# Kernel optimization log

Hardware: AMD Instinct MI355X
Metric: run time of the kernel (lower is better)

## Reference

```python
import jax
import jax.numpy as jnp
from jax import lax
import numpy as np

# module hyperparameters (match init_kwargs)
IN_C, OUT_C = 32, 64
K, STRIDE, PAD, DIL = 3, 1, 1, 1
GRID_SIZE, ORDER = 5, 3
GRID_LO, GRID_HI = -1.0, 1.0
SCALE_SPLINE = 1.0
EPS = 1e-8


def _knot_grid():
    # grid = arange(-order, grid_size+order+1) * h + lo ; length = grid_size + 2*order + 1 = 12
    h = (GRID_HI - GRID_LO) / GRID_SIZE
    return jnp.arange(-ORDER, GRID_SIZE + ORDER + 1, dtype=jnp.float32) * h + GRID_LO


def _bspline_bases(x):
    """Cox-de Boor recursion. x: (N, P) -> bases: (N, P, GRID_SIZE+ORDER)."""
    grid = _knot_grid()
    xe = x[..., None]  # (N, P, 1)
    bases = ((xe >= grid[:-1]) & (xe < grid[1:])).astype(x.dtype)  # (N, P, 11)
    for k in range(1, ORDER + 1):
        left_den = jnp.maximum(grid[k:-1] - grid[:-(k + 1)], EPS)
        right_den = jnp.maximum(grid[k + 1:] - grid[1:-k], EPS)
        bases = ((xe - grid[:-(k + 1)]) / left_den * bases[..., :-1]
                 + (grid[k + 1:] - xe) / right_den * bases[..., 1:])
    return bases  # (N, P, 8)


def setup_inputs() -> dict:
    key = jax.random.key(0)
    k1, k2, k3 = jax.random.split(key, 3)
    x = jax.random.normal(k1, (4, IN_C, 56, 56), dtype=jnp.float32)
    base_weight = jax.random.normal(k2, (OUT_C, IN_C, K, K), dtype=jnp.float32) * 0.05
    spline_weight = jax.random.normal(k3, (OUT_C, IN_C * K * K, GRID_SIZE + ORDER), dtype=jnp.float32) * 0.05
    spline_scaler = jnp.ones((OUT_C,), dtype=jnp.float32)
    return {"x": x, "base_weight": base_weight,
            "spline_weight": spline_weight, "spline_scaler": spline_scaler}


def reference(x, base_weight, spline_weight, spline_scaler):
    B, C, H, W = x.shape
    pad = [(PAD, PAD), (PAD, PAD)]
    # base path: conv2d -> SiLU
    base_conv = lax.conv_general_dilated(
        x, base_weight, window_strides=(STRIDE, STRIDE), padding=pad,
        rhs_dilation=(DIL, DIL), dimension_numbers=("NCHW", "OIHW", "NCHW"))
    base_out = jax.nn.silu(base_conv)

    # unfold: (B, C*K*K, oh, ow) with torch Unfold channel ordering (c, kh, kw)
    patches = lax.conv_general_dilated_patches(
        x, filter_shape=(K, K), window_strides=(STRIDE, STRIDE), padding=pad,
        rhs_dilation=(DIL, DIL))
    oh, ow = patches.shape[2], patches.shape[3]
    num_patches = oh * ow
    # (B*num_patches, C*K*K)
    pf = patches.reshape(B, C * K * K, num_patches).transpose(0, 2, 1).reshape(-1, C * K * K)

    bases = _bspline_bases(pf)  # (N, P, F)
    # contract patch-dim and basis-dim against spline weights
    spl = jnp.einsum("npf,opf->no", bases, spline_weight) * spline_scaler  # (N, O)
    spl = spl.reshape(B, num_patches, OUT_C).transpose(0, 2, 1).reshape(B, OUT_C, oh, ow)
    return base_out + SCALE_SPLINE * spl
```

## Files before the change

### kernel.cpp

```cpp
#include <hip/hip_runtime.h>
#include <math.h>


typedef __attribute__((ext_vector_type(8))) short bf16x8;
typedef __attribute__((ext_vector_type(4))) float f32x4;

#define MFMA16(a, b, c) __builtin_amdgcn_mfma_f32_16x16x32_bf16((a), (b), (c), 0, 0, 0)

__device__ __forceinline__ unsigned short f2bf(float f) {
    unsigned u = __builtin_bit_cast(unsigned, f);
    u = (u + 0x7fffu + ((u >> 16) & 1u)) >> 16;
    return (unsigned short)u;
}

__device__ __forceinline__ void eval_bases(float v, float bs[8]) {
    #pragma unroll
    for (int i = 0; i < 8; ++i) bs[i] = 0.0f;
    float t = (v + 2.2f) * 2.5f;
    if (t >= 0.0f && t < 11.0f) {
        int j = (int)t;
        if (j > 10) j = 10;
        float knot = (float)(j - 3) * 0.4f - 1.0f;
        float u  = (v - knot) * 2.5f;
        float um = 1.0f - u;
        float u2 = u * u, u3 = u2 * u;
        const float s6 = 1.0f / 6.0f;
        float w0 = um * um * um * s6;
        float w1 = (3.0f * u3 - 6.0f * u2 + 4.0f) * s6;
        float w2 = (-3.0f * u3 + 3.0f * u2 + 3.0f * u + 1.0f) * s6;
        float w3 = u3 * s6;
        int i0 = j - 3;
        if (i0 >= 0)               bs[i0]     = w0;
        if (i0 + 1 >= 0 && i0 < 7) bs[i0 + 1] = w1;
        if (i0 + 2 >= 0 && i0 < 6) bs[i0 + 2] = w2;
        if (i0 + 3 <= 7)           bs[i0 + 3] = w3;
    }
}

__global__ __launch_bounds__(256)
void cvt_swz_kernel(const float* __restrict__ ws, const float* __restrict__ wb,
                    unsigned short* __restrict__ wst, unsigned short* __restrict__ wbt) {
    int i = blockIdx.x * 256 + threadIdx.x;
    if (i < 147456) {
        int j = i & 7, l = (i >> 3) & 63, t = i >> 9;
        int S = t % 72, nq = t / 72;
        int oc = nq * 16 + (l & 15);
        int k  = S * 32 + (l >> 4) * 8 + j;
        wst[i] = f2bf(ws[oc * 2304 + k]);
    } else {
        int i2 = i - 147456;
        if (i2 < 18432) {
            int j = i2 & 7, l = (i2 >> 3) & 63, t = i2 >> 9;
            int s = t % 9, nq = t / 9;
            int oc = nq * 16 + (l & 15);
            int k  = s * 32 + (l >> 4) * 8 + j;
            wbt[i2] = f2bf(wb[oc * 288 + k]);
        }
    }
}

__global__ __launch_bounds__(512)
void kan_mfma_kernel(const float* __restrict__ x,
                     const float* __restrict__ sc,
                     const unsigned short* __restrict__ wst,
                     const unsigned short* __restrict__ wbt,
                     float* __restrict__ out) {
    __shared__ unsigned short smem[24832];
    unsigned short* sb    = smem;
    unsigned short* patch = smem + 15360;

    const int tid = threadIdx.x;
    const int bx  = blockIdx.x;
    const int b   = bx / 98;
    const int r   = bx - b * 98;
    const int ty  = r / 7;
    const int tx  = r - ty * 7;
    const int h0  = ty * 4, w0 = tx * 8;

    const int lane = tid & 63;
    const int wv   = tid >> 6;
    const int nq   = wv & 3;
    const int kh   = wv >> 2;
    const int ml   = lane & 15;
    const int kg   = lane >> 4;
    const int py0  = ml >> 3, px0 = ml & 7;

    float vv[4];
    #pragma unroll
    for (int j = 0; j < 4; ++j) {
        int i = tid + j * 512;
        float val = 0.0f;
        if (i < 1920) {
            int c  = i / 60;
            int hp = i - c * 60;
            int hy = hp / 10;
            int hx = hp - hy * 10;
            int hh = h0 + hy - 1, ww = w0 + hx - 1;
            if ((unsigned)hh < 56u && (unsigned)ww < 56u)
                val = x[((b * 32 + c) * 56 + hh) * 56 + ww];
        }
        vv[j] = val;
    }
    #pragma unroll
    for (int j = 0; j < 4; ++j) {
        int i = tid + j * 512;
        if (i < 1920) {
            int c  = i / 60;
            int hp = i - c * 60;
            int hy = hp / 10;
            int hx = hp - hy * 10;
            float bs[8];
            eval_bases(vv[j], bs);
            bf16x8 pk;
            #pragma unroll
            for (int j2 = 0; j2 < 8; ++j2) pk[j2] = (short)f2bf(bs[j2]);
            *reinterpret_cast<bf16x8*>(&sb[i * 8]) = pk;
            unsigned short xb = f2bf(vv[j]);
            #pragma unroll
            for (int dkh = 0; dkh < 3; ++dkh) {
                int py = hy - dkh;
                if ((unsigned)py < 4u) {
                    #pragma unroll
                    for (int dkw = 0; dkw < 3; ++dkw) {
                        int px = hx - dkw;
                        if ((unsigned)px < 8u)
                            patch[(py * 8 + px) * 296 + c * 9 + dkh * 3 + dkw] = xb;
                    }
                }
            }
        }
    }
    __syncthreads();

    int aoff[9];
    #pragma unroll
    for (int u = 0; u < 9; ++u) {
        int tt  = 4 * u + kg;
        int dc  = tt / 9;
        int tap = tt - dc * 9;
        int th  = tap / 3;
        int tw  = tap - th * 3;
        aoff[u] = (dc * 60 + (py0 + th) * 10 + (px0 + tw)) * 8;
    }

    f32x4 accS0 = {0.f, 0.f, 0.f, 0.f};
    f32x4 accS1 = {0.f, 0.f, 0.f, 0.f};
    f32x4 accB0 = {0.f, 0.f, 0.f, 0.f};
    f32x4 accB1 = {0.f, 0.f, 0.f, 0.f};

    const unsigned short* bp = wst + ((nq * 72 + kh * 36) * 64 + lane) * 8;
    int cbase = kh * 4 * 1920;
    for (int g = 0; g < 4; ++g) {
        #pragma unroll
        for (int u = 0; u < 9; ++u) {
            bf16x8 a0 = *reinterpret_cast<const bf16x8*>(&sb[cbase + aoff[u]]);
            bf16x8 a1 = *reinterpret_cast<const bf16x8*>(&sb[cbase + aoff[u] + 160]);
            bf16x8 bw = *reinterpret_cast<const bf16x8*>(bp + (g * 9 + u) * 512);
            accS0 = MFMA16(a0, bw, accS0);
            accS1 = MFMA16(a1, bw, accS1);
        }
        cbase += 1920;
    }

    {
        const unsigned short* ap0 = patch + ml * 296 + kg * 8;
        const unsigned short* ap1 = ap0 + 16 * 296;
        const unsigned short* bbp = wbt + (nq * 9 * 64 + lane) * 8;
        const int sbeg = kh ? 5 : 0;
        const int send = kh ? 9 : 5;
        for (int s = sbeg; s < send; ++s) {
            bf16x8 a0 = *reinterpret_cast<const bf16x8*>(ap0 + s * 32);
            bf16x8 a1 = *reinterpret_cast<const bf16x8*>(ap1 + s * 32);
            bf16x8 bw = *reinterpret_cast<const bf16x8*>(bbp + s * 512);
            accB0 = MFMA16(a0, bw, accB0);
            accB1 = MFMA16(a1, bw, accB1);
        }
    }

    __syncthreads();
    float* red = reinterpret_cast<float*>(smem);
    const int idx = nq * 64 + lane;
    if (kh) {
        #pragma unroll
        for (int w = 0; w < 4; ++w) red[(0  + w) * 260 + idx] = accS0[w];
        #pragma unroll
        for (int w = 0; w < 4; ++w) red[(4  + w) * 260 + idx] = accS1[w];
        #pragma unroll
        for (int w = 0; w < 4; ++w) red[(8  + w) * 260 + idx] = accB0[w];
        #pragma unroll
        for (int w = 0; w < 4; ++w) red[(12 + w) * 260 + idx] = accB1[w];
    }
    __syncthreads();
    if (!kh) {
        #pragma unroll
        for (int w = 0; w < 4; ++w) accS0[w] += red[(0  + w) * 260 + idx];
        #pragma unroll
        for (int w = 0; w < 4; ++w) accS1[w] += red[(4  + w) * 260 + idx];
        #pragma unroll
        for (int w = 0; w < 4; ++w) accB0[w] += red[(8  + w) * 260 + idx];
        #pragma unroll
        for (int w = 0; w < 4; ++w) accB1[w] += red[(12 + w) * 260 + idx];

        const int oc  = nq * 16 + ml;
        const float scv = sc[oc];
        #pragma unroll
        for (int f = 0; f < 2; ++f) {
            const int rowb = f * 16 + kg * 4;
            const int py   = rowb >> 3;
            const int pxb  = rowb & 7;
            float* ob = out + ((b * 64 + oc) * 56 + h0 + py) * 56 + w0 + pxb;
            f32x4 aB = f ? accB1 : accB0;
            f32x4 aS = f ? accS1 : accS0;
            f32x4 res;
            #pragma unroll
            for (int reg = 0; reg < 4; ++reg) {
                float bv = aB[reg];
                float si = bv / (1.0f + __expf(-bv));
                res[reg] = si + scv * aS[reg];
            }
            *reinterpret_cast<f32x4*>(ob) = res;
        }
    }
}

extern "C" void kernel_launch(void* const* d_in, const int* in_sizes, int n_in,
                              void* d_out, int out_size, void* d_ws, size_t ws_size,
                              hipStream_t stream) {
    const float* x  = (const float*)d_in[0];
    const float* wb = (const float*)d_in[1];
    const float* ws = (const float*)d_in[2];
    const float* sc = (const float*)d_in[3];
    float* out = (float*)d_out;

    unsigned short* wst = (unsigned short*)d_ws;
    unsigned short* wbt = wst + 147456;

    cvt_swz_kernel<<<648, 256, 0, stream>>>(ws, wb, wst, wbt);
    kan_mfma_kernel<<<392, 512, 0, stream>>>(x, sc, wst, wbt, out);
}
```

Measured before the change: 77.60 us.

## Double spatial tile to 8x8 and use channel-major halo for base conv

Each block now covers an 8x8 output tile instead of 4x8, halving the grid and doubling M-rows per wave, so every loaded B-weight fragment feeds four MFMAs instead of two. The explicit 3x3 patch buffer for the base convolution is replaced by a channel-contiguous halo array indexed per tap, and the base weights are reordered tap-major to match. This lowers global weight traffic and removes scattered LDS patch writes, at the cost of more LDS per block and only 196 blocks, which is below one block per CU on a 256-CU part.

```diff
diff --git a/kernel.cpp b/kernel.cpp
--- a/kernel.cpp
+++ b/kernel.cpp
@@ -53,8 +53,8 @@
             int j = i2 & 7, l = (i2 >> 3) & 63, t = i2 >> 9;
             int s = t % 9, nq = t / 9;
             int oc = nq * 16 + (l & 15);
-            int k  = s * 32 + (l >> 4) * 8 + j;
-            wbt[i2] = f2bf(wb[oc * 288 + k]);
+            int c  = (l >> 4) * 8 + j;
+            wbt[i2] = f2bf(wb[oc * 288 + c * 9 + s]);
         }
     }
 }
@@ -65,17 +65,17 @@
                      const unsigned short* __restrict__ wst,
                      const unsigned short* __restrict__ wbt,
                      float* __restrict__ out) {
-    __shared__ unsigned short smem[24832];
-    unsigned short* sb    = smem;
-    unsigned short* patch = smem + 15360;
+    __shared__ unsigned short smem[29600];
+    unsigned short* sb = smem;
+    unsigned short* xh = smem + 25600;
 
     const int tid = threadIdx.x;
     const int bx  = blockIdx.x;
-    const int b   = bx / 98;
-    const int r   = bx - b * 98;
+    const int b   = bx / 49;
+    const int r   = bx - b * 49;
     const int ty  = r / 7;
     const int tx  = r - ty * 7;
-    const int h0  = ty * 4, w0 = tx * 8;
+    const int h0  = ty * 8, w0 = tx * 8;
 
     const int lane = tid & 63;
     const int wv   = tid >> 6;
@@ -85,14 +85,14 @@
     const int kg   = lane >> 4;
     const int py0  = ml >> 3, px0 = ml & 7;
 
-    float vv[4];
-    #pragma unroll
-    for (int j = 0; j < 4; ++j) {
+    float vv[7];
+    #pragma unroll
+    for (int j = 0; j < 7; ++j) {
         int i = tid + j * 512;
         float val = 0.0f;
-        if (i < 1920) {
-            int c  = i / 60;
-            int hp = i - c * 60;
+        if (i < 3200) {
+            int c  = i / 100;
+            int hp = i - c * 100;
             int hy = hp / 10;
             int hx = hp - hy * 10;
             int hh = h0 + hy - 1, ww = w0 + hx - 1;
@@ -102,32 +102,18 @@
         vv[j] = val;
     }
     #pragma unroll
-    for (int j = 0; j < 4; ++j) {
+    for (int j = 0; j < 7; ++j) {
         int i = tid + j * 512;
-        if (i < 1920) {
-            int c  = i / 60;
-            int hp = i - c * 60;
-            int hy = hp / 10;
-            int hx = hp - hy * 10;
+        if (i < 3200) {
+            int c  = i / 100;
+            int hp = i - c * 100;
             float bs[8];
             eval_bases(vv[j], bs);
             bf16x8 pk;
             #pragma unroll
             for (int j2 = 0; j2 < 8; ++j2) pk[j2] = (short)f2bf(bs[j2]);
             *reinterpret_cast<bf16x8*>(&sb[i * 8]) = pk;
-            unsigned short xb = f2bf(vv[j]);
-            #pragma unroll
-            for (int dkh = 0; dkh < 3; ++dkh) {
-                int py = hy - dkh;
-                if ((unsigned)py < 4u) {
-                    #pragma unroll
-                    for (int dkw = 0; dkw < 3; ++dkw) {
-                        int px = hx - dkw;
-                        if ((unsigned)px < 8u)
-                            patch[(py * 8 + px) * 296 + c * 9 + dkh * 3 + dkw] = xb;
-                    }
-                }
-            }
+            xh[hp * 40 + c] = f2bf(vv[j]);
         }
     }
     __syncthreads();
@@ -140,40 +126,41 @@
         int tap = tt - dc * 9;
         int th  = tap / 3;
         int tw  = tap - th * 3;
-        aoff[u] = (dc * 60 + (py0 + th) * 10 + (px0 + tw)) * 8;
-    }
-
-    f32x4 accS0 = {0.f, 0.f, 0.f, 0.f};
-    f32x4 accS1 = {0.f, 0.f, 0.f, 0.f};
-    f32x4 accB0 = {0.f, 0.f, 0.f, 0.f};
-    f32x4 accB1 = {0.f, 0.f, 0.f, 0.f};
+        aoff[u] = (dc * 100 + (py0 + th) * 10 + (px0 + tw)) * 8;
+    }
+
+    f32x4 aS[4] = {{0,0,0,0},{0,0,0,0},{0,0,0,0},{0,0,0,0}};
+    f32x4 aB[4] = {{0,0,0,0},{0,0,0,0},{0,0,0,0},{0,0,0,0}};
 
     const unsigned short* bp = wst + ((nq * 72 + kh * 36) * 64 + lane) * 8;
-    int cbase = kh * 4 * 1920;
+    int cbase = kh * 12800;
     for (int g = 0; g < 4; ++g) {
         #pragma unroll
         for (int u = 0; u < 9; ++u) {
-            bf16x8 a0 = *reinterpret_cast<const bf16x8*>(&sb[cbase + aoff[u]]);
-            bf16x8 a1 = *reinterpret_cast<const bf16x8*>(&sb[cbase + aoff[u] + 160]);
             bf16x8 bw = *reinterpret_cast<const bf16x8*>(bp + (g * 9 + u) * 512);
-            accS0 = MFMA16(a0, bw, accS0);
-            accS1 = MFMA16(a1, bw, accS1);
-        }
-        cbase += 1920;
+            #pragma unroll
+            for (int f = 0; f < 4; ++f) {
+                bf16x8 a = *reinterpret_cast<const bf16x8*>(&sb[cbase + aoff[u] + f * 160]);
+                aS[f] = MFMA16(a, bw, aS[f]);
+            }
+        }
+        cbase += 3200;
     }
 
     {
-        const unsigned short* ap0 = patch + ml * 296 + kg * 8;
-        const unsigned short* ap1 = ap0 + 16 * 296;
         const unsigned short* bbp = wbt + (nq * 9 * 64 + lane) * 8;
         const int sbeg = kh ? 5 : 0;
         const int send = kh ? 9 : 5;
         for (int s = sbeg; s < send; ++s) {
-            bf16x8 a0 = *reinterpret_cast<const bf16x8*>(ap0 + s * 32);
-            bf16x8 a1 = *reinterpret_cast<const bf16x8*>(ap1 + s * 32);
+            int th = (s * 11) >> 5;
+            int tw = s - 3 * th;
             bf16x8 bw = *reinterpret_cast<const bf16x8*>(bbp + s * 512);
-            accB0 = MFMA16(a0, bw, accB0);
-            accB1 = MFMA16(a1, bw, accB1);
+            int xa = ((py0 + th) * 10 + (px0 + tw)) * 40 + kg * 8;
+            #pragma unroll
+            for (int f = 0; f < 4; ++f) {
+                bf16x8 a = *reinterpret_cast<const bf16x8*>(&xh[xa + f * 800]);
+                aB[f] = MFMA16(a, bw, aB[f]);
+            }
         }
     }
 
@@ -182,41 +169,38 @@
     const int idx = nq * 64 + lane;
     if (kh) {
         #pragma unroll
-        for (int w = 0; w < 4; ++w) red[(0  + w) * 260 + idx] = accS0[w];
-        #pragma unroll
-        for (int w = 0; w < 4; ++w) red[(4  + w) * 260 + idx] = accS1[w];
-        #pragma unroll
-        for (int w = 0; w < 4; ++w) red[(8  + w) * 260 + idx] = accB0[w];
-        #pragma unroll
-        for (int w = 0; w < 4; ++w) red[(12 + w) * 260 + idx] = accB1[w];
+        for (int f = 0; f < 4; ++f)
+            #pragma unroll
+            for (int w = 0; w < 4; ++w) red[(f * 4 + w) * 260 + idx] = aS[f][w];
+        #pragma unroll
+        for (int f = 0; f < 4; ++f)
+            #pragma unroll
+            for (int w = 0; w < 4; ++w) red[((16 + f * 4) + w) * 260 + idx] = aB[f][w];
     }
     __syncthreads();
     if (!kh) {
         #pragma unroll
-        for (int w = 0; w < 4; ++w) accS0[w] += red[(0  + w) * 260 + idx];
-        #pragma unroll
-        for (int w = 0; w < 4; ++w) accS1[w] += red[(4  + w) * 260 + idx];
-        #pragma unroll
-        for (int w = 0; w < 4; ++w) accB0[w] += red[(8  + w) * 260 + idx];
-        #pragma unroll
-        for (int w = 0; w < 4; ++w) accB1[w] += red[(12 + w) * 260 + idx];
+        for (int f = 0; f < 4; ++f)
+            #pragma unroll
+            for (int w = 0; w < 4; ++w) aS[f][w] += red[(f * 4 + w) * 260 + idx];
+        #pragma unroll
+        for (int f = 0; f < 4; ++f)
+            #pragma unroll
+            for (int w = 0; w < 4; ++w) aB[f][w] += red[((16 + f * 4) + w) * 260 + idx];
 
         const int oc  = nq * 16 + ml;
         const float scv = sc[oc];
         #pragma unroll
-        for (int f = 0; f < 2; ++f) {
-            const int rowb = f * 16 + kg * 4;
-            const int py   = rowb >> 3;
-            const int pxb  = rowb & 7;
+        for (int f = 0; f < 4; ++f) {
+            const int py  = f * 2 + (kg >> 1);
+            const int pxb = (kg & 1) * 4;
             float* ob = out + ((b * 64 + oc) * 56 + h0 + py) * 56 + w0 + pxb;
-            f32x4 aB = f ? accB1 : accB0;
-            f32x4 aS = f ? accS1 : accS0;
             f32x4 res;
             #pragma unroll
             for (int reg = 0; reg < 4; ++reg) {
-                float bv = aB[reg];
+                float bv = aB[f][reg];
                 float si = bv / (1.0f + __expf(-bv));
-                res[reg] = si + scv * aS[reg];
+                res[reg] = si + scv * aS[f][reg];
             }
             *reinterpret_cast<f32x4*>(ob) = res;
         }
@@ -236,5 +220,5 @@
     unsigned short* wbt = wst + 147456;
 
     cvt_swz_kernel<<<648, 256, 0, stream>>>(ws, wb, wst, wbt);
-    kan_mfma_kernel<<<392, 512, 0, stream>>>(x, sc, wst, wbt, out);
-}
+    kan_mfma_kernel<<<196, 512, 0, stream>>>(x, sc, wst, wbt, out);
+}
```

New measurement: 73.17 us. -5.7%, faster.
